# Kernel tuning notes

Measured on AMD Instinct MI355X. Metric: run time of the kernel, lower is better.

## Reference

```python
import jax, jax.numpy as jnp
import numpy as np

N, F, F_, H = 8192, 512, 64, 8
NEG = -1e10

def setup_inputs() -> dict:
    key = jax.random.key(0)
    k1, k2, k3, k4 = jax.random.split(key, 4)
    X = jax.random.normal(k1, (N, F), dtype=jnp.float32)
    A = jax.random.randint(k2, (N, N), 0, 2).astype(jnp.float32)  # dense 0/1 adjacency
    kernels = jax.random.normal(k3, (H, F, F_), dtype=jnp.float32) * 0.05
    attn_kernels = jax.random.normal(k4, (H, 2 * F_), dtype=jnp.float32) * 0.05
    return {"X": X, "A": A, "kernels": kernels, "attn_kernels": attn_kernels}

def reference(X, A, kernels, attn_kernels):
    # Per-head linear transform: [H, N, F_]
    WX = jnp.einsum('nf,hfo->hno', X, kernels)
    a1 = attn_kernels[:, :F_]   # [H, F_] acts on source (row) node
    a2 = attn_kernels[:, F_:]   # [H, F_] acts on target (col) node
    # score[h,i,j] = a1_h . WX[h,i] + a2_h . WX[h,j]  (outer sum, no N^2*2F_ tensor)
    s1 = jnp.einsum('hno,ho->hn', WX, a1)  # [H, N]
    s2 = jnp.einsum('hno,ho->hn', WX, a2)  # [H, N]
    scores = s1[:, :, None] + s2[:, None, :]  # [H, N, N]
    # adjacency mask: A==0 -> -1e10 (note: original has no LeakyReLU)
    masked = jnp.where(A[None, :, :] == 0.0, scores + NEG, scores)
    attn = jax.nn.softmax(masked, axis=-1)  # [H, N, N]
    # dropout is identity at inference (Keras Dropout without training=True)
    feats = jnp.einsum('hnm,hmo->hno', attn, WX)  # [H, N, F_]
    feats = jax.nn.relu(feats)  # concat reduction applies activation per head
    out = jnp.transpose(feats, (1, 0, 2)).reshape(N, H * F_)  # concat heads
    return out
```

## Files before the change

kernel.cpp:

```cpp
#include <hip/hip_runtime.h>
#include <cstdint>

#define NN 8192
#define FF 512
#define FO 64
#define NH 8
#define LDYE 520
#define YPART (8192 * 520)
#define SPLITK 2


typedef __attribute__((ext_vector_type(8))) __bf16 bf16x8;
typedef __attribute__((ext_vector_type(4))) float f32x4;
typedef __attribute__((ext_vector_type(4))) int i32x4;
typedef __attribute__((ext_vector_type(8))) int i32x8;

__device__ __forceinline__ unsigned short f2bf(float f) {
    unsigned int u = __float_as_uint(f);
    u += 0x7fffu + ((u >> 16) & 1u);
    return (unsigned short)(u >> 16);
}

__device__ __forceinline__ void gload16(const void* g, void* l) {
    __builtin_amdgcn_global_load_lds(
        (const __attribute__((address_space(1))) unsigned int*)g,
        (__attribute__((address_space(3))) unsigned int*)l,
        16, 0, 0);
}

__global__ __launch_bounds__(256) void k_prep(const float* __restrict__ X,
                                              const float* __restrict__ Kw,
                                              unsigned short* __restrict__ Xb,
                                              unsigned short* __restrict__ Ktb) {
    const int b = blockIdx.x;
    const int t = threadIdx.x;
    if (b < 2048) {
        size_t base = ((size_t)b * 256 + t) * 8;
        float4 a = *(const float4*)(X + base);
        float4 c = *(const float4*)(X + base + 4);
        ushort4 o0, o1;
        o0.x = f2bf(a.x); o0.y = f2bf(a.y); o0.z = f2bf(a.z); o0.w = f2bf(a.w);
        o1.x = f2bf(c.x); o1.y = f2bf(c.y); o1.z = f2bf(c.z); o1.w = f2bf(c.w);
        *(ushort4*)(Xb + base) = o0;
        *(ushort4*)(Xb + base + 4) = o1;
    } else {
        int h = b - 2048;
        for (int e = t; e < FF * FO; e += 256) {
            int o = e >> 9, f = e & 511;
            Ktb[(size_t)h * FF * FO + e] = f2bf(Kw[(size_t)h * FF * FO + (size_t)f * FO + o]);
        }
    }
}

union WxSmem {
    struct { unsigned short Xs[4096]; unsigned short Ks[2048]; } s;
    unsigned char Vs[64][144];
};
union FusedSmem {
    WxSmem wx;
    unsigned char Ls[64][272];
};

__global__ __launch_bounds__(256) void k_fused(const float* __restrict__ A,
                                               unsigned char* __restrict__ Ab,
                                               const unsigned short* __restrict__ Xb,
                                               const unsigned short* __restrict__ Ktb,
                                               const float* __restrict__ Aw,
                                               unsigned char* __restrict__ Vt) {
    __shared__ FusedSmem fsm;
    const int id = blockIdx.x;
    const int t = threadIdx.x;

    if (id >= 512) {
        const int cid = id - 512;
        const int rt = cid >> 5;
        const int cb = cid & 31;
        const float* src = A + ((size_t)rt << 19) + ((size_t)cb << 8);
#pragma unroll
        for (int p = 0; p < 16; ++p) {
            int row = p * 4 + (t >> 6);
            int col = (t & 63) * 4;
            uint4 v = *(const uint4*)(src + ((size_t)row << 13) + col);
            unsigned o = ((v.x >> 22) & 0x38u) | (((v.y >> 22) & 0x38u) << 8) |
                         (((v.z >> 22) & 0x38u) << 16) | (((v.w >> 22) & 0x38u) << 24);
            *(unsigned*)&fsm.Ls[row][col] = o;
        }
        __syncthreads();
        unsigned char* dst = Ab + (((size_t)rt * 512 + (size_t)cb * 16) << 10);
#pragma unroll
        for (int j = 0; j < 4; ++j) {
            int g = t + 256 * j;
            int row = g & 63, k16l = g >> 6;
            *(uint4*)(dst + ((size_t)g << 4)) = *(const uint4*)&fsm.Ls[row][k16l * 16];
        }
        return;
    }

    WxSmem& sm = fsm.wx;
    const int n0 = (id & 63) * 128;
    const int h = id >> 6;
    const int lane = t & 63, w = t >> 6;
    const int quad = lane >> 4, l15 = lane & 15;

    const unsigned short* xS0 = Xb + (size_t)(n0 + (t & 127)) * FF + (t >> 7) * 8;
    const unsigned short* xS1 = Xb + (size_t)(n0 + ((t + 256) & 127)) * FF + ((t + 256) >> 7) * 8;
    unsigned short* xD0 = sm.s.Xs + t * 8;
    unsigned short* xD1 = sm.s.Xs + (t + 256) * 8;
    const unsigned short* kS = Ktb + (size_t)h * FF * FO + (size_t)(t & 63) * FF + (t >> 6) * 8;
    unsigned short* kD = sm.s.Ks + t * 8;

    const bf16x8* aF[2];
    const bf16x8* bF[4];
    for (int i = 0; i < 2; ++i)
        aF[i] = (const bf16x8*)(sm.s.Xs + (size_t)(quad * 128 + w * 32 + i * 16 + l15) * 8);
    for (int j = 0; j < 4; ++j)
        bF[j] = (const bf16x8*)(sm.s.Ks + (size_t)(quad * 64 + j * 16 + l15) * 8);

    f32x4 acc[2][4] = {};
    for (int f0 = 0; f0 < FF; f0 += 32) {
        gload16(xS0 + f0, xD0);
        gload16(xS1 + f0, xD1);
        gload16(kS + f0, kD);
        __syncthreads();
        bf16x8 av[2], bv[4];
        for (int i = 0; i < 2; ++i) av[i] = aF[i][0];
        for (int j = 0; j < 4; ++j) bv[j] = bF[j][0];
        for (int i = 0; i < 2; ++i)
            for (int j = 0; j < 4; ++j)
                acc[i][j] = __builtin_amdgcn_mfma_f32_16x16x32_bf16(av[i], bv[j], acc[i][j], 0, 0, 0);
        __syncthreads();
    }

    float a2v[4];
    for (int j = 0; j < 4; ++j) a2v[j] = Aw[h * 128 + 64 + j * 16 + l15];
    float ex[2][4];
    for (int i = 0; i < 2; ++i)
        for (int r = 0; r < 4; ++r) {
            float p = acc[i][0][r] * a2v[0] + acc[i][1][r] * a2v[1]
                    + acc[i][2][r] * a2v[2] + acc[i][3][r] * a2v[3];
            p += __shfl_xor(p, 1);
            p += __shfl_xor(p, 2);
            p += __shfl_xor(p, 4);
            p += __shfl_xor(p, 8);
            ex[i][r] = __expf(p);
        }

    for (int i = 0; i < 2; ++i)
        for (int j = 0; j < 4; ++j) {
            int rowb = w * 32 + i * 16 + quad * 4;
            int col = j * 16 + l15;
            unsigned u = __builtin_amdgcn_cvt_pk_fp8_f32(
                ex[i][0] * acc[i][j][0], ex[i][1] * acc[i][j][1], 0, false);
            u = __builtin_amdgcn_cvt_pk_fp8_f32(
                ex[i][2] * acc[i][j][2], ex[i][3] * acc[i][j][3], (int)u, true);
            *(unsigned*)&sm.Vs[col][rowb] = u;
        }
    __syncthreads();
    for (int j2 = 0; j2 < 2; ++j2) {
        int vid = t + j2 * 256;
        int o = vid >> 3, k16o = vid & 7;
        size_t H = (size_t)((n0 >> 4) + k16o) * 640 + h * 64 + o;
        *(uint4*)(Vt + (H << 4)) = *(const uint4*)&sm.Vs[o][k16o * 16];
    }
    if (l15 == 0) {
        for (int i = 0; i < 2; ++i)
            for (int r = 0; r < 4; ++r) {
                int row = w * 32 + i * 16 + quad * 4 + r;
                unsigned u = __builtin_amdgcn_cvt_pk_fp8_f32(ex[i][r], ex[i][r], 0, false);
                size_t H = (size_t)((n0 >> 4) + (row >> 4)) * 640 + 512 + h;
                Vt[(H << 4) + (row & 15)] = (unsigned char)(u & 0xff);
            }
    }
}

__global__ __launch_bounds__(256, 5) void k_gemm(const unsigned char* __restrict__ Ab,
                                                 const unsigned char* __restrict__ Vt,
                                                 float* __restrict__ Y) {
    __shared__ unsigned char As[8192];
    __shared__ unsigned char Bs[16384];
    const int t = threadIdx.x;
    const int id = blockIdx.x;
    const int xcd = id & 7;
    const int u = id >> 3;
    const int ct = u % 5;
    const int rp = (u / 5) * 8 + xcd;
    const int rt = rp & 127;
    const int part = rp >> 7;
    const int ks0 = part * 32;
    const int ks1 = ks0 + 32;

    const unsigned char* aS = Ab + ((size_t)rt << 19) + (size_t)t * 16;
    unsigned char* aD0 = As + t * 16;
    unsigned char* aD1 = As + t * 16 + 4096;
    const unsigned char* bS[4];
    unsigned char* bD[4];
#pragma unroll
    for (int j = 0; j < 4; ++j) {
        int g = t + 256 * j;
        bS[j] = Vt + (size_t)((g >> 7) * 640 + ct * 128 + (g & 127)) * 16;
        bD[j] = Bs + g * 16;
    }

    const int lane = t & 63;
    const int w = t >> 6;
    const int wm = w >> 1, wn = w & 1;
    const int quad = lane >> 4, l15 = lane & 15;

    int aOff[2], bOff[4];
#pragma unroll
    for (int i = 0; i < 2; ++i)
        aOff[i] = quad * 2048 + (wm * 32 + i * 16 + l15) * 16;
#pragma unroll
    for (int j = 0; j < 4; ++j)
        bOff[j] = quad * 4096 + (wn * 64 + j * 16 + l15) * 16;

    f32x4 acc[2][4] = {};

    for (int ks = ks0; ks < ks1; ++ks) {
        const size_t koA = (size_t)ks << 13;
        const size_t koB = (size_t)ks * 81920;
        gload16(aS + koA, aD0);
        gload16(aS + koA + 4096, aD1);
#pragma unroll
        for (int j = 0; j < 4; ++j) gload16(bS[j] + koB, bD[j]);
        __syncthreads();
        i32x8 av[2];
#pragma unroll
        for (int i = 0; i < 2; ++i) {
            i32x4 lo = *(const i32x4*)(As + aOff[i]);
            i32x4 hi = *(const i32x4*)(As + aOff[i] + 1024);
            av[i] = __builtin_shufflevector(lo, hi, 0, 1, 2, 3, 4, 5, 6, 7);
        }
#pragma unroll
        for (int j = 0; j < 4; ++j) {
            i32x4 lo = *(const i32x4*)(Bs + bOff[j]);
            i32x4 hi = *(const i32x4*)(Bs + bOff[j] + 2048);
            i32x8 bv = __builtin_shufflevector(lo, hi, 0, 1, 2, 3, 4, 5, 6, 7);
            acc[0][j] = __builtin_amdgcn_mfma_scale_f32_16x16x128_f8f6f4(
                av[0], bv, acc[0][j], 0, 0, 0, 0x7f7f7f7f, 0, 0x7f7f7f7f);
            acc[1][j] = __builtin_amdgcn_mfma_scale_f32_16x16x128_f8f6f4(
                av[1], bv, acc[1][j], 0, 0, 0, 0x7f7f7f7f, 0, 0x7f7f7f7f);
        }
        __syncthreads();
    }

    float* Yp = Y + (size_t)part * YPART;
    for (int i = 0; i < 2; ++i) {
        int row = rt * 64 + wm * 32 + i * 16 + quad * 4;
        for (int j = 0; j < 4; ++j) {
            int col = ct * 128 + wn * 64 + j * 16 + l15;
            if (col < 520) {
                for (int r = 0; r < 4; ++r)
                    Yp[(size_t)(row + r) * LDYE + col] = acc[i][j][r];
            }
        }
    }
}

__global__ __launch_bounds__(256) void k_epi(const float* __restrict__ Y,
                                             float* __restrict__ out) {
    int idx = blockIdx.x * 256 + threadIdx.x;
    int n = idx >> 7;
    int c = (idx & 127) * 4;
    int h = c >> 6;
    float4 u = {0.f, 0.f, 0.f, 0.f};
    float den = 0.f;
    const float* yp = Y + (size_t)n * LDYE;
#pragma unroll
    for (int p = 0; p < SPLITK; ++p) {
        float4 v = *(const float4*)(yp + c);
        u.x += v.x; u.y += v.y; u.z += v.z; u.w += v.w;
        den += yp[512 + h];
        yp += (size_t)YPART;
    }
    float inv = 1.0f / den;
    float4 o;
    o.x = fmaxf(u.x * inv, 0.f);
    o.y = fmaxf(u.y * inv, 0.f);
    o.z = fmaxf(u.z * inv, 0.f);
    o.w = fmaxf(u.w * inv, 0.f);
    *(float4*)(out + (size_t)n * 512 + c) = o;
}

extern "C" void kernel_launch(void* const* d_in, const int* in_sizes, int n_in,
                              void* d_out, int out_size, void* d_ws, size_t ws_size,
                              hipStream_t stream) {
    const float* X  = (const float*)d_in[0];
    const float* A  = (const float*)d_in[1];
    const float* Kw = (const float*)d_in[2];
    const float* Aw = (const float*)d_in[3];
    float* out = (float*)d_out;
    char* ws = (char*)d_ws;
    unsigned char* Ab = (unsigned char*)ws;
    unsigned char* Vt = (unsigned char*)(ws + (size_t)67108864);
    float* Yb = (float*)(ws + (size_t)67108864 + (size_t)5242880);
    unsigned short* Xb = (unsigned short*)Yb;
    unsigned short* Ktb = Xb + (size_t)NN * FF;

    k_prep<<<dim3(2056), dim3(256), 0, stream>>>(X, Kw, Xb, Ktb);
    k_fused<<<dim3(4608), dim3(256), 0, stream>>>(A, Ab, Xb, Ktb, Aw, Vt);
    k_gemm<<<dim3(1280), dim3(256), 0, stream>>>(Ab, Vt, Yb);
    k_epi<<<dim3(4096), dim3(256), 0, stream>>>(Yb, out);
}
```

Before: 462.8 us.

## Drop split-K and fuse softmax normalization epilogue into fp8 GEMM

Removes the split-K partial-sum buffer and the separate epilogue kernel. Each GEMM block now runs the full K range and computes the denominator column tile with one extra MFMA per step. It then normalizes, applies ReLU and writes the output directly. This saves the fp32 intermediate write/read and a kernel launch, but the grid shrinks from 1280 to 512 blocks with a 64-step K loop, which reduces parallelism and latency hiding; the denominator MFMA is redundantly repeated in all blocks.

```diff
diff --git a/kernel.cpp b/kernel.cpp
--- a/kernel.cpp
+++ b/kernel.cpp
@@ -5,9 +5,6 @@
 #define FF 512
 #define FO 64
 #define NH 8
-#define LDYE 520
-#define YPART (8192 * 520)
-#define SPLITK 2
 
 
 typedef __attribute__((ext_vector_type(8))) __bf16 bf16x8;
@@ -173,21 +170,17 @@
     }
 }
 
-__global__ __launch_bounds__(256, 5) void k_gemm(const unsigned char* __restrict__ Ab,
+__global__ __launch_bounds__(256, 2) void k_gemm(const unsigned char* __restrict__ Ab,
                                                  const unsigned char* __restrict__ Vt,
-                                                 float* __restrict__ Y) {
+                                                 float* __restrict__ out) {
     __shared__ unsigned char As[8192];
-    __shared__ unsigned char Bs[16384];
+    __shared__ unsigned char Bs[18432];
     const int t = threadIdx.x;
     const int id = blockIdx.x;
     const int xcd = id & 7;
     const int u = id >> 3;
-    const int ct = u % 5;
-    const int rp = (u / 5) * 8 + xcd;
-    const int rt = rp & 127;
-    const int part = rp >> 7;
-    const int ks0 = part * 32;
-    const int ks1 = ks0 + 32;
+    const int ct = u & 3;
+    const int rt = (u >> 2) * 8 + xcd;
 
     const unsigned char* aS = Ab + ((size_t)rt << 19) + (size_t)t * 16;
     unsigned char* aD0 = As + t * 16;
@@ -200,6 +193,8 @@
         bS[j] = Vt + (size_t)((g >> 7) * 640 + ct * 128 + (g & 127)) * 16;
         bD[j] = Bs + g * 16;
     }
+    const unsigned char* dS = Vt + (size_t)((t >> 4) * 640 + 512 + (t & 15)) * 16;
+    unsigned char* dD = Bs + 16384 + t * 16;
 
     const int lane = t & 63;
     const int w = t >> 6;
@@ -213,16 +208,19 @@
 #pragma unroll
     for (int j = 0; j < 4; ++j)
         bOff[j] = quad * 4096 + (wn * 64 + j * 16 + l15) * 16;
+    const int dOff = 16384 + quad * 512 + l15 * 16;
 
     f32x4 acc[2][4] = {};
-
-    for (int ks = ks0; ks < ks1; ++ks) {
+    f32x4 accD[2] = {};
+
+    for (int ks = 0; ks < 64; ++ks) {
         const size_t koA = (size_t)ks << 13;
         const size_t koB = (size_t)ks * 81920;
         gload16(aS + koA, aD0);
         gload16(aS + koA + 4096, aD1);
 #pragma unroll
         for (int j = 0; j < 4; ++j) gload16(bS[j] + koB, bD[j]);
+        if (t < 128) gload16(dS + koB, dD);
         __syncthreads();
         i32x8 av[2];
 #pragma unroll
@@ -230,6 +228,15 @@
             i32x4 lo = *(const i32x4*)(As + aOff[i]);
             i32x4 hi = *(const i32x4*)(As + aOff[i] + 1024);
             av[i] = __builtin_shufflevector(lo, hi, 0, 1, 2, 3, 4, 5, 6, 7);
+        }
+        {
+            i32x4 lo = *(const i32x4*)(Bs + dOff);
+            i32x4 hi = *(const i32x4*)(Bs + dOff + 256);
+            i32x8 dv = __builtin_shufflevector(lo, hi, 0, 1, 2, 3, 4, 5, 6, 7);
+            accD[0] = __builtin_amdgcn_mfma_scale_f32_16x16x128_f8f6f4(
+                av[0], dv, accD[0], 0, 0, 0, 0x7f7f7f7f, 0, 0x7f7f7f7f);
+            accD[1] = __builtin_amdgcn_mfma_scale_f32_16x16x128_f8f6f4(
+                av[1], dv, accD[1], 0, 0, 0, 0x7f7f7f7f, 0, 0x7f7f7f7f);
         }
 #pragma unroll
         for (int j = 0; j < 4; ++j) {
@@ -244,42 +251,22 @@
         __syncthreads();
     }
 
-    float* Yp = Y + (size_t)part * YPART;
+    const int h = ct * 2 + wn;
     for (int i = 0; i < 2; ++i) {
         int row = rt * 64 + wm * 32 + i * 16 + quad * 4;
+        float inv[4];
+#pragma unroll
+        for (int r = 0; r < 4; ++r) {
+            float d = __shfl(accD[i][r], quad * 16 + h);
+            inv[r] = 1.0f / d;
+        }
         for (int j = 0; j < 4; ++j) {
             int col = ct * 128 + wn * 64 + j * 16 + l15;
-            if (col < 520) {
-                for (int r = 0; r < 4; ++r)
-                    Yp[(size_t)(row + r) * LDYE + col] = acc[i][j][r];
-            }
-        }
-    }
-}
-
-__global__ __launch_bounds__(256) void k_epi(const float* __restrict__ Y,
-                                             float* __restrict__ out) {
-    int idx = blockIdx.x * 256 + threadIdx.x;
-    int n = idx >> 7;
-    int c = (idx & 127) * 4;
-    int h = c >> 6;
-    float4 u = {0.f, 0.f, 0.f, 0.f};
-    float den = 0.f;
-    const float* yp = Y + (size_t)n * LDYE;
-#pragma unroll
-    for (int p = 0; p < SPLITK; ++p) {
-        float4 v = *(const float4*)(yp + c);
-        u.x += v.x; u.y += v.y; u.z += v.z; u.w += v.w;
-        den += yp[512 + h];
-        yp += (size_t)YPART;
-    }
-    float inv = 1.0f / den;
-    float4 o;
-    o.x = fmaxf(u.x * inv, 0.f);
-    o.y = fmaxf(u.y * inv, 0.f);
-    o.z = fmaxf(u.z * inv, 0.f);
-    o.w = fmaxf(u.w * inv, 0.f);
-    *(float4*)(out + (size_t)n * 512 + c) = o;
+#pragma unroll
+            for (int r = 0; r < 4; ++r)
+                out[(size_t)(row + r) * 512 + col] = fmaxf(acc[i][j][r] * inv[r], 0.f);
+        }
+    }
 }
 
 extern "C" void kernel_launch(void* const* d_in, const int* in_sizes, int n_in,
@@ -293,12 +280,10 @@
     char* ws = (char*)d_ws;
     unsigned char* Ab = (unsigned char*)ws;
     unsigned char* Vt = (unsigned char*)(ws + (size_t)67108864);
-    float* Yb = (float*)(ws + (size_t)67108864 + (size_t)5242880);
-    unsigned short* Xb = (unsigned short*)Yb;
+    unsigned short* Xb = (unsigned short*)(ws + (size_t)67108864 + (size_t)5242880);
     unsigned short* Ktb = Xb + (size_t)NN * FF;
 
     k_prep<<<dim3(2056), dim3(256), 0, stream>>>(X, Kw, Xb, Ktb);
     k_fused<<<dim3(4608), dim3(256), 0, stream>>>(A, Ab, Xb, Ktb, Aw, Vt);
-    k_gemm<<<dim3(1280), dim3(256), 0, stream>>>(Ab, Vt, Yb);
-    k_epi<<<dim3(4096), dim3(256), 0, stream>>>(Yb, out);
-}
+    k_gemm<<<dim3(512), dim3(256), 0, stream>>>(Ab, Vt, out);
+}
```

Result: no change. 466.5 us (+0.8%).
